# Optimization experiments

Measured on AMD Instinct MI355X. Metric: run time of the kernel, lower is better.

The kernel has to match this reference:

```python
import jax, jax.numpy as jnp
import numpy as np


def _gru_cell(x, h, W_ih, W_hh, b_ih, b_hh):
    # torch.nn.GRUCell math; gate order (r, z, n). x: [.,D] or [1,D] (broadcast), h: [E,D]
    gi = x @ W_ih.T + b_ih            # [., 3D]
    gh = h @ W_hh.T + b_hh            # [E, 3D]
    i_r, i_z, i_n = jnp.split(gi, 3, axis=-1)
    h_r, h_z, h_n = jnp.split(gh, 3, axis=-1)
    r = jax.nn.sigmoid(i_r + h_r)
    z = jax.nn.sigmoid(i_z + h_z)
    n = jnp.tanh(i_n + r * h_n)
    return (1.0 - z) * n + z * h


def setup_inputs() -> dict:
    D = 256          # num_embed_units
    E = 200000       # neighbor edges of the seed
    N = E + 1        # nodes in the sampled subgraph (seed is node E)
    V = 500000       # entity vocab
    R = 1000         # relation vocab
    key = jax.random.key(0)
    ks = jax.random.split(key, 14)
    s = 1.0 / np.sqrt(D)  # torch default init bound
    inp = {
        "encoder_output": jax.random.normal(ks[0], (1, D), jnp.float32),
        "sample_mask": jax.random.normal(ks[1], (1, D), jnp.float32),
        "entity_table": jax.random.normal(ks[2], (V, D), jnp.float32) * 0.02,
        "rel_table": jax.random.normal(ks[3], (R, D), jnp.float32) * 0.02,
        "W_ih": jax.random.uniform(ks[4], (3 * D, D), jnp.float32, -s, s),
        "W_hh": jax.random.uniform(ks[5], (3 * D, D), jnp.float32, -s, s),
        "b_ih": jax.random.uniform(ks[6], (3 * D,), jnp.float32, -s, s),
        "b_hh": jax.random.uniform(ks[7], (3 * D,), jnp.float32, -s, s),
        "sub_W": jax.random.uniform(ks[8], (D, D), jnp.float32, -s, s),
        "sub_b": jax.random.uniform(ks[9], (D,), jnp.float32, -s, s),
        "obj_W": jax.random.uniform(ks[10], (D, D), jnp.float32, -s, s),
        "obj_b": jax.random.uniform(ks[11], (D,), jnp.float32, -s, s),
        "rel_ids": jax.random.randint(ks[12], (E,), 0, R, jnp.int64 if jax.config.jax_enable_x64 else jnp.int32),
        "tail_ids": jnp.arange(E, dtype=jnp.int32),
        "tails_state": jax.random.randint(ks[13], (E,), 0, 2, jnp.int32),
        "origin_ids": jax.random.randint(jax.random.fold_in(key, 99), (E,), 0, V, jnp.int32),
        "seed": E,
        "num_nodes": N,
    }
    return inp


def reference(encoder_output, sample_mask, entity_table, rel_table, W_ih, W_hh, b_ih, b_hh,
              sub_W, sub_b, obj_W, obj_b, rel_ids, tail_ids, tails_state, origin_ids, seed, num_nodes):
    D = encoder_output.shape[-1]
    # seed_state == 0 branch: sub = tanh(Linear(sample_mask))
    sub = jnp.tanh(sample_mask @ sub_W.T + sub_b)                      # [1, D]
    r0 = _gru_cell(encoder_output, sub, W_ih, W_hh, b_ih, b_hh)        # [1, D]
    # vectorized per-edge GRUCell: input r0 (broadcast), hidden = relation embedding
    rel_emb = rel_table[rel_ids]                                       # [E, D]
    rj = _gru_cell(r0, rel_emb, W_ih, W_hh, b_ih, b_hh)                # [E, D]
    obj = jnp.tanh(rj @ obj_W.T + obj_b)                               # [E, D]
    # tails with state==1 get their pretrained entity embedding instead
    from_table = entity_table[origin_ids]                              # [E, D]
    tail_vals = jnp.where((tails_state == 1)[:, None], from_table, obj)
    ent = jnp.zeros((num_nodes, D), dtype=encoder_output.dtype)
    ent = ent.at[seed].set(sub[0])
    ent = ent.at[tail_ids].set(tail_vals)
    return ent
```

## Files before the change

### kernel.cpp

```cpp
#include <hip/hip_runtime.h>
#include <hip/hip_bf16.h>

typedef unsigned short u16;
using bf16x8 = __attribute__((ext_vector_type(8))) short;
using f32x4  = __attribute__((ext_vector_type(4))) float;

__device__ __forceinline__ u16 f2b(float f) {
    unsigned u = __float_as_uint(f);
    return (u16)((u + 0x7fffu + ((u >> 16) & 1u)) >> 16);
}
__device__ __forceinline__ float sigm(float x) { return 1.f / (1.f + expf(-x)); }

__device__ __forceinline__ bf16x8 pack8(const float* p) {
    float4 a = *(const float4*)p, b = *(const float4*)(p + 4);
    bf16x8 r;
    r[0] = (short)f2b(a.x); r[1] = (short)f2b(a.y);
    r[2] = (short)f2b(a.z); r[3] = (short)f2b(a.w);
    r[4] = (short)f2b(b.x); r[5] = (short)f2b(b.y);
    r[6] = (short)f2b(b.z); r[7] = (short)f2b(b.w);
    return r;
}

__device__ __forceinline__ float dot64(const float* __restrict__ w, const float* s) {
    float acc = 0.f;
    #pragma unroll
    for (int i = 0; i < 16; ++i) {
        float4 v = ((const float4*)w)[i];
        acc += v.x * s[i*4] + v.y * s[i*4+1] + v.z * s[i*4+2] + v.w * s[i*4+3];
    }
    return acc;
}

__global__ __launch_bounds__(1024)
void k1_head(const float* __restrict__ enc, const float* __restrict__ mask,
             const float* __restrict__ W_ih, const float* __restrict__ W_hh,
             const float* __restrict__ b_ih, const float* __restrict__ b_hh,
             const float* __restrict__ sub_W, const float* __restrict__ sub_b,
             float* __restrict__ gi1, float* __restrict__ out,
             const int* __restrict__ seed_p)
{
    __shared__ float enc_s[256], mask_s[256], sub_s[256], r0_s[256];
    __shared__ float gi_s[768], gh_s[768];
    __shared__ float pA[1024], pB[1024];
    const int tid = threadIdx.x;
    if (tid < 256)       mask_s[tid]      = mask[tid];
    else if (tid < 512)  enc_s[tid - 256] = enc[tid - 256];
    __syncthreads();

    const int d = tid >> 2, g = tid & 3;

    pA[tid] = dot64(sub_W + d * 256 + g * 64, mask_s + g * 64);
    __syncthreads();
    if (tid < 256) {
        float s = tanhf(pA[4*tid] + pA[4*tid+1] + pA[4*tid+2] + pA[4*tid+3] + sub_b[tid]);
        sub_s[tid] = s;
        out[(size_t)seed_p[0] * 256 + tid] = s;
    }
    __syncthreads();

    for (int r = 0; r < 3; ++r) {
        const int j = r * 256 + d;
        pA[tid] = dot64(W_ih + (size_t)j * 256 + g * 64, enc_s + g * 64);
        pB[tid] = dot64(W_hh + (size_t)j * 256 + g * 64, sub_s + g * 64);
        __syncthreads();
        if (tid < 256) {
            const int jj = r * 256 + tid;
            gi_s[jj] = pA[4*tid] + pA[4*tid+1] + pA[4*tid+2] + pA[4*tid+3] + b_ih[jj];
            gh_s[jj] = pB[4*tid] + pB[4*tid+1] + pB[4*tid+2] + pB[4*tid+3] + b_hh[jj];
        }
        __syncthreads();
    }
    if (tid < 256) {
        float rr = sigm(gi_s[tid] + gh_s[tid]);
        float zz = sigm(gi_s[256 + tid] + gh_s[256 + tid]);
        float nn = tanhf(gi_s[512 + tid] + rr * gh_s[512 + tid]);
        r0_s[tid] = (1.f - zz) * nn + zz * sub_s[tid];
    }
    __syncthreads();
    for (int r = 0; r < 3; ++r) {
        const int j = r * 256 + d;
        pA[tid] = dot64(W_ih + (size_t)j * 256 + g * 64, r0_s + g * 64);
        __syncthreads();
        if (tid < 256) {
            const int jj = r * 256 + tid;
            gi1[jj] = pA[4*tid] + pA[4*tid+1] + pA[4*tid+2] + pA[4*tid+3] + b_ih[jj];
        }
        __syncthreads();
    }
}

__global__ __launch_bounds__(64)
void k2_gh(const float* __restrict__ rel_table, const float* __restrict__ W_hh,
           const float* __restrict__ b_hh, float* __restrict__ gh, int R)
{
    const int l = threadIdx.x, m = l & 15, q = l >> 4;
    const int tt = blockIdx.y, jt = blockIdx.x;
    int trow = tt * 16 + m; if (trow >= R) trow = R - 1;
    const float* ab = rel_table + (size_t)trow * 256 + q * 8;
    const float* bb = W_hh + (size_t)(jt * 16 + m) * 256 + q * 8;
    f32x4 acc = {0.f, 0.f, 0.f, 0.f};
    #pragma unroll
    for (int kk = 0; kk < 8; ++kk) {
        bf16x8 a = pack8(ab + kk * 32);
        bf16x8 b = pack8(bb + kk * 32);
        acc = __builtin_amdgcn_mfma_f32_16x16x32_bf16(a, b, acc, 0, 0, 0);
    }
    const int col = jt * 16 + m;
    const float bias = b_hh[col];
    #pragma unroll
    for (int i = 0; i < 4; ++i) {
        const int row = tt * 16 + q * 4 + i;
        if (row < R) gh[(size_t)row * 768 + col] = acc[i] + bias;
    }
}

__global__ __launch_bounds__(256)
void k2_comb(const float* __restrict__ gh, const float* __restrict__ gi1,
             const float* __restrict__ rel_table, u16* __restrict__ rj)
{
    const int t = blockIdx.x, dd = threadIdx.x;
    const float gr = gh[(size_t)t * 768 + dd];
    const float gz = gh[(size_t)t * 768 + 256 + dd];
    const float gn = gh[(size_t)t * 768 + 512 + dd];
    const float r = sigm(gi1[dd] + gr);
    const float z = sigm(gi1[256 + dd] + gz);
    const float n = tanhf(gi1[512 + dd] + r * gn);
    const float h = rel_table[(size_t)t * 256 + dd];
    rj[(size_t)t * 256 + dd] = f2b((1.f - z) * n + z * h);
}

__global__ __launch_bounds__(64)
void k2_obj(const u16* __restrict__ rj, const float* __restrict__ obj_W,
            const float* __restrict__ obj_b, float* __restrict__ obj, int R)
{
    const int l = threadIdx.x, m = l & 15, q = l >> 4;
    const int tt = blockIdx.y, jt = blockIdx.x;
    int trow = tt * 16 + m; if (trow >= R) trow = R - 1;
    const u16* ab = rj + (size_t)trow * 256 + q * 8;
    const float* bb = obj_W + (size_t)(jt * 16 + m) * 256 + q * 8;
    f32x4 acc = {0.f, 0.f, 0.f, 0.f};
    #pragma unroll
    for (int kk = 0; kk < 8; ++kk) {
        bf16x8 a = *(const bf16x8*)(ab + kk * 32);
        bf16x8 b = pack8(bb + kk * 32);
        acc = __builtin_amdgcn_mfma_f32_16x16x32_bf16(a, b, acc, 0, 0, 0);
    }
    const int col = jt * 16 + m;
    const float bias = obj_b[col];
    #pragma unroll
    for (int i = 0; i < 4; ++i) {
        const int row = tt * 16 + q * 4 + i;
        if (row < R) obj[(size_t)row * 256 + col] = tanhf(acc[i] + bias);
    }
}

__global__ __launch_bounds__(256)
void k3_scatter(const float* __restrict__ entity, const float* __restrict__ obj,
                const int* __restrict__ rel_ids, const int* __restrict__ tail_ids,
                const int* __restrict__ state, const int* __restrict__ origin,
                float* __restrict__ out, int E)
{
    const long long gidx = (long long)blockIdx.x * 256 + threadIdx.x;
    const int e = (int)(gidx >> 6);
    if (e >= E) return;
    const int c = ((int)gidx & 63) * 4;
    const float* src = (state[e] == 1) ? entity + (size_t)origin[e] * 256
                                       : obj + (size_t)rel_ids[e] * 256;
    *(float4*)(out + (size_t)tail_ids[e] * 256 + c) = *(const float4*)(src + c);
}

extern "C" void kernel_launch(void* const* d_in, const int* in_sizes, int n_in,
                              void* d_out, int out_size, void* d_ws, size_t ws_size,
                              hipStream_t stream)
{
    const float* enc       = (const float*)d_in[0];
    const float* mask      = (const float*)d_in[1];
    const float* entity    = (const float*)d_in[2];
    const float* rel_table = (const float*)d_in[3];
    const float* W_ih      = (const float*)d_in[4];
    const float* W_hh      = (const float*)d_in[5];
    const float* b_ih      = (const float*)d_in[6];
    const float* b_hh      = (const float*)d_in[7];
    const float* sub_W     = (const float*)d_in[8];
    const float* sub_b     = (const float*)d_in[9];
    const float* obj_W     = (const float*)d_in[10];
    const float* obj_b     = (const float*)d_in[11];
    const int* rel_ids     = (const int*)d_in[12];
    const int* tail_ids    = (const int*)d_in[13];
    const int* state       = (const int*)d_in[14];
    const int* origin      = (const int*)d_in[15];
    const int* seed_p      = (const int*)d_in[16];
    float* out = (float*)d_out;

    const int E = in_sizes[12];
    const int R = in_sizes[3] / 256;

    float* gi1 = (float*)d_ws;
    float* gh  = gi1 + 1024;
    u16*   rj  = (u16*)(gh + (size_t)R * 768);
    float* obj = (float*)(rj + (size_t)R * 256);

    k1_head<<<1, 1024, 0, stream>>>(enc, mask, W_ih, W_hh, b_ih, b_hh,
                                    sub_W, sub_b, gi1, out, seed_p);
    dim3 g_gh(48, (R + 15) / 16);
    k2_gh<<<g_gh, 64, 0, stream>>>(rel_table, W_hh, b_hh, gh, R);
    k2_comb<<<R, 256, 0, stream>>>(gh, gi1, rel_table, rj);
    dim3 g_obj(16, (R + 15) / 16);
    k2_obj<<<g_obj, 64, 0, stream>>>(rj, obj_W, obj_b, obj, R);
    const int blocks = (int)(((long long)E * 64 + 255) / 256);
    k3_scatter<<<blocks, 256, 0, stream>>>(entity, obj, rel_ids, tail_ids,
                                           state, origin, out, E);
}
```

Before: 819.9 us.

## Split single-block GRU head into multi-block kernels, fuse gh with gate combine

Replaces the single 1024-thread head kernel with three small multi-block kernels so the seed GRU matvecs spread across several CUs instead of one. It also computes r, z and n gate MFMAs together in one kernel and applies the GRU combine in registers, removing the R x 768 gh round trip and the separate combine launch. The scatter now uses nontemporal stores for the large output. It adds two extra kernel launches for the head chain.

```diff
diff --git a/kernel.cpp b/kernel.cpp
--- a/kernel.cpp
+++ b/kernel.cpp
@@ -4,6 +4,7 @@
 typedef unsigned short u16;
 using bf16x8 = __attribute__((ext_vector_type(8))) short;
 using f32x4  = __attribute__((ext_vector_type(4))) float;
+using f4     = __attribute__((ext_vector_type(4))) float;
 
 __device__ __forceinline__ u16 f2b(float f) {
     unsigned u = __float_as_uint(f);
@@ -31,102 +32,121 @@
     return acc;
 }
 
-__global__ __launch_bounds__(1024)
-void k1_head(const float* __restrict__ enc, const float* __restrict__ mask,
-             const float* __restrict__ W_ih, const float* __restrict__ W_hh,
-             const float* __restrict__ b_ih, const float* __restrict__ b_hh,
-             const float* __restrict__ sub_W, const float* __restrict__ sub_b,
-             float* __restrict__ gi1, float* __restrict__ out,
-             const int* __restrict__ seed_p)
-{
-    __shared__ float enc_s[256], mask_s[256], sub_s[256], r0_s[256];
-    __shared__ float gi_s[768], gh_s[768];
-    __shared__ float pA[1024], pB[1024];
+__global__ __launch_bounds__(256)
+void k1a_sub_gi0(const float* __restrict__ enc, const float* __restrict__ mask,
+                 const float* __restrict__ W_ih, const float* __restrict__ b_ih,
+                 const float* __restrict__ sub_W, const float* __restrict__ sub_b,
+                 float* __restrict__ sub_ws, float* __restrict__ gi0,
+                 float* __restrict__ out, const int* __restrict__ seed_p)
+{
+    __shared__ float x_s[256];
+    __shared__ float pA[256];
+    const int b = blockIdx.x;
+    const bool is_sub = (b < 4);
     const int tid = threadIdx.x;
-    if (tid < 256)       mask_s[tid]      = mask[tid];
-    else if (tid < 512)  enc_s[tid - 256] = enc[tid - 256];
-    __syncthreads();
-
-    const int d = tid >> 2, g = tid & 3;
-
-    pA[tid] = dot64(sub_W + d * 256 + g * 64, mask_s + g * 64);
-    __syncthreads();
-    if (tid < 256) {
-        float s = tanhf(pA[4*tid] + pA[4*tid+1] + pA[4*tid+2] + pA[4*tid+3] + sub_b[tid]);
-        sub_s[tid] = s;
-        out[(size_t)seed_p[0] * 256 + tid] = s;
-    }
-    __syncthreads();
-
-    for (int r = 0; r < 3; ++r) {
-        const int j = r * 256 + d;
-        pA[tid] = dot64(W_ih + (size_t)j * 256 + g * 64, enc_s + g * 64);
-        pB[tid] = dot64(W_hh + (size_t)j * 256 + g * 64, sub_s + g * 64);
-        __syncthreads();
-        if (tid < 256) {
-            const int jj = r * 256 + tid;
-            gi_s[jj] = pA[4*tid] + pA[4*tid+1] + pA[4*tid+2] + pA[4*tid+3] + b_ih[jj];
-            gh_s[jj] = pB[4*tid] + pB[4*tid+1] + pB[4*tid+2] + pB[4*tid+3] + b_hh[jj];
+    x_s[tid] = is_sub ? mask[tid] : enc[tid];
+    __syncthreads();
+    const int t = tid >> 2, g = tid & 3;
+    if (is_sub) {
+        const int i = b * 64 + t;
+        pA[tid] = dot64(sub_W + (size_t)i * 256 + g * 64, x_s + g * 64);
+    } else {
+        const int j = (b - 4) * 64 + t;
+        pA[tid] = dot64(W_ih + (size_t)j * 256 + g * 64, x_s + g * 64);
+    }
+    __syncthreads();
+    if (tid < 64) {
+        float v = pA[4*tid] + pA[4*tid+1] + pA[4*tid+2] + pA[4*tid+3];
+        if (is_sub) {
+            const int i = b * 64 + tid;
+            float s = tanhf(v + sub_b[i]);
+            sub_ws[i] = s;
+            out[(size_t)seed_p[0] * 256 + i] = s;
+        } else {
+            const int j = (b - 4) * 64 + tid;
+            gi0[j] = v + b_ih[j];
         }
-        __syncthreads();
-    }
-    if (tid < 256) {
-        float rr = sigm(gi_s[tid] + gh_s[tid]);
-        float zz = sigm(gi_s[256 + tid] + gh_s[256 + tid]);
-        float nn = tanhf(gi_s[512 + tid] + rr * gh_s[512 + tid]);
-        r0_s[tid] = (1.f - zz) * nn + zz * sub_s[tid];
-    }
-    __syncthreads();
-    for (int r = 0; r < 3; ++r) {
-        const int j = r * 256 + d;
-        pA[tid] = dot64(W_ih + (size_t)j * 256 + g * 64, r0_s + g * 64);
-        __syncthreads();
-        if (tid < 256) {
-            const int jj = r * 256 + tid;
-            gi1[jj] = pA[4*tid] + pA[4*tid+1] + pA[4*tid+2] + pA[4*tid+3] + b_ih[jj];
-        }
-        __syncthreads();
+    }
+}
+
+__global__ __launch_bounds__(256)
+void k1b_gh0(const float* __restrict__ sub_ws, const float* __restrict__ W_hh,
+             const float* __restrict__ b_hh, float* __restrict__ gh0)
+{
+    __shared__ float x_s[256];
+    __shared__ float pA[256];
+    const int tid = threadIdx.x;
+    x_s[tid] = sub_ws[tid];
+    __syncthreads();
+    const int t = tid >> 2, g = tid & 3;
+    const int j = blockIdx.x * 64 + t;
+    pA[tid] = dot64(W_hh + (size_t)j * 256 + g * 64, x_s + g * 64);
+    __syncthreads();
+    if (tid < 64) {
+        const int jj = blockIdx.x * 64 + tid;
+        gh0[jj] = pA[4*tid] + pA[4*tid+1] + pA[4*tid+2] + pA[4*tid+3] + b_hh[jj];
+    }
+}
+
+__global__ __launch_bounds__(256)
+void k1c_gi1(const float* __restrict__ sub_ws, const float* __restrict__ gi0,
+             const float* __restrict__ gh0, const float* __restrict__ W_ih,
+             const float* __restrict__ b_ih, float* __restrict__ gi1)
+{
+    __shared__ float r0_s[256];
+    __shared__ float pA[256];
+    const int tid = threadIdx.x;
+    {
+        float rr = sigm(gi0[tid]       + gh0[tid]);
+        float zz = sigm(gi0[256 + tid] + gh0[256 + tid]);
+        float nn = tanhf(gi0[512 + tid] + rr * gh0[512 + tid]);
+        r0_s[tid] = (1.f - zz) * nn + zz * sub_ws[tid];
+    }
+    __syncthreads();
+    const int t = tid >> 2, g = tid & 3;
+    const int j = blockIdx.x * 64 + t;
+    pA[tid] = dot64(W_ih + (size_t)j * 256 + g * 64, r0_s + g * 64);
+    __syncthreads();
+    if (tid < 64) {
+        const int jj = blockIdx.x * 64 + tid;
+        gi1[jj] = pA[4*tid] + pA[4*tid+1] + pA[4*tid+2] + pA[4*tid+3] + b_ih[jj];
     }
 }
 
 __global__ __launch_bounds__(64)
-void k2_gh(const float* __restrict__ rel_table, const float* __restrict__ W_hh,
-           const float* __restrict__ b_hh, float* __restrict__ gh, int R)
+void k2_ghcomb(const float* __restrict__ rel_table, const float* __restrict__ W_hh,
+               const float* __restrict__ b_hh, const float* __restrict__ gi1,
+               u16* __restrict__ rj, int R)
 {
     const int l = threadIdx.x, m = l & 15, q = l >> 4;
     const int tt = blockIdx.y, jt = blockIdx.x;
     int trow = tt * 16 + m; if (trow >= R) trow = R - 1;
+    const int col = jt * 16 + m;
     const float* ab = rel_table + (size_t)trow * 256 + q * 8;
-    const float* bb = W_hh + (size_t)(jt * 16 + m) * 256 + q * 8;
-    f32x4 acc = {0.f, 0.f, 0.f, 0.f};
+    const float* b0 = W_hh + (size_t)(col      ) * 256 + q * 8;
+    const float* b1 = W_hh + (size_t)(col + 256) * 256 + q * 8;
+    const float* b2 = W_hh + (size_t)(col + 512) * 256 + q * 8;
+    f32x4 aR = {0.f,0.f,0.f,0.f}, aZ = {0.f,0.f,0.f,0.f}, aN = {0.f,0.f,0.f,0.f};
     #pragma unroll
     for (int kk = 0; kk < 8; ++kk) {
         bf16x8 a = pack8(ab + kk * 32);
-        bf16x8 b = pack8(bb + kk * 32);
-        acc = __builtin_amdgcn_mfma_f32_16x16x32_bf16(a, b, acc, 0, 0, 0);
-    }
-    const int col = jt * 16 + m;
-    const float bias = b_hh[col];
+        aR = __builtin_amdgcn_mfma_f32_16x16x32_bf16(a, pack8(b0 + kk * 32), aR, 0, 0, 0);
+        aZ = __builtin_amdgcn_mfma_f32_16x16x32_bf16(a, pack8(b1 + kk * 32), aZ, 0, 0, 0);
+        aN = __builtin_amdgcn_mfma_f32_16x16x32_bf16(a, pack8(b2 + kk * 32), aN, 0, 0, 0);
+    }
+    const float gr = gi1[col], gz = gi1[256 + col], gn = gi1[512 + col];
+    const float br = b_hh[col], bz = b_hh[256 + col], bn = b_hh[512 + col];
     #pragma unroll
     for (int i = 0; i < 4; ++i) {
         const int row = tt * 16 + q * 4 + i;
-        if (row < R) gh[(size_t)row * 768 + col] = acc[i] + bias;
-    }
-}
-
-__global__ __launch_bounds__(256)
-void k2_comb(const float* __restrict__ gh, const float* __restrict__ gi1,
-             const float* __restrict__ rel_table, u16* __restrict__ rj)
-{
-    const int t = blockIdx.x, dd = threadIdx.x;
-    const float gr = gh[(size_t)t * 768 + dd];
-    const float gz = gh[(size_t)t * 768 + 256 + dd];
-    const float gn = gh[(size_t)t * 768 + 512 + dd];
-    const float r = sigm(gi1[dd] + gr);
-    const float z = sigm(gi1[256 + dd] + gz);
-    const float n = tanhf(gi1[512 + dd] + r * gn);
-    const float h = rel_table[(size_t)t * 256 + dd];
-    rj[(size_t)t * 256 + dd] = f2b((1.f - z) * n + z * h);
+        if (row < R) {
+            const float h = rel_table[(size_t)row * 256 + col];
+            const float r = sigm(gr + aR[i] + br);
+            const float z = sigm(gz + aZ[i] + bz);
+            const float n = tanhf(gn + r * (aN[i] + bn));
+            rj[(size_t)row * 256 + col] = f2b((1.f - z) * n + z * h);
+        }
+    }
 }
 
 __global__ __launch_bounds__(64)
@@ -166,7 +186,8 @@
     const int c = ((int)gidx & 63) * 4;
     const float* src = (state[e] == 1) ? entity + (size_t)origin[e] * 256
                                        : obj + (size_t)rel_ids[e] * 256;
-    *(float4*)(out + (size_t)tail_ids[e] * 256 + c) = *(const float4*)(src + c);
+    f4 v = *(const f4*)(src + c);
+    __builtin_nontemporal_store(v, (f4*)(out + (size_t)tail_ids[e] * 256 + c));
 }
 
 extern "C" void kernel_launch(void* const* d_in, const int* in_sizes, int n_in,
@@ -195,18 +216,24 @@
     const int E = in_sizes[12];
     const int R = in_sizes[3] / 256;
 
-    float* gi1 = (float*)d_ws;
-    float* gh  = gi1 + 1024;
-    u16*   rj  = (u16*)(gh + (size_t)R * 768);
-    float* obj = (float*)(rj + (size_t)R * 256);
-
-    k1_head<<<1, 1024, 0, stream>>>(enc, mask, W_ih, W_hh, b_ih, b_hh,
-                                    sub_W, sub_b, gi1, out, seed_p);
-    dim3 g_gh(48, (R + 15) / 16);
-    k2_gh<<<g_gh, 64, 0, stream>>>(rel_table, W_hh, b_hh, gh, R);
-    k2_comb<<<R, 256, 0, stream>>>(gh, gi1, rel_table, rj);
+    float* ws     = (float*)d_ws;
+    float* sub_ws = ws;
+    float* gi0    = ws + 256;
+    float* gh0    = ws + 1024;
+    float* gi1    = ws + 1792;
+    u16*   rj     = (u16*)(ws + 2560);
+    float* obj    = (float*)((char*)rj + (size_t)R * 256 * 2);
+
+    k1a_sub_gi0<<<16, 256, 0, stream>>>(enc, mask, W_ih, b_ih, sub_W, sub_b,
+                                        sub_ws, gi0, out, seed_p);
+    k1b_gh0<<<12, 256, 0, stream>>>(sub_ws, W_hh, b_hh, gh0);
+    k1c_gi1<<<12, 256, 0, stream>>>(sub_ws, gi0, gh0, W_ih, b_ih, gi1);
+
+    dim3 g_ghc(16, (R + 15) / 16);
+    k2_ghcomb<<<g_ghc, 64, 0, stream>>>(rel_table, W_hh, b_hh, gi1, rj, R);
     dim3 g_obj(16, (R + 15) / 16);
     k2_obj<<<g_obj, 64, 0, stream>>>(rj, obj_W, obj_b, obj, R);
+
     const int blocks = (int)(((long long)E * 64 + 255) / 256);
     k3_scatter<<<blocks, 256, 0, stream>>>(entity, obj, rel_ids, tail_ids,
                                            state, origin, out, E);
```

New measurement: 713.8 us. 1.15x faster.
